# Kernel tuning notes

Measured on AMD Instinct MI355X. Metric: run time of the kernel, lower is better.

The kernel has to match this reference:

```python
import jax, jax.numpy as jnp
import numpy as np

B, S, H = 32, 2048, 1024

def setup_inputs() -> dict:
    key = jax.random.key(0)
    k1, k2, k3, k4, k5, k6 = jax.random.split(key, 6)
    return {
        "query": jax.random.normal(k1, (B, 1, H), dtype=jnp.float32),
        "keys": jax.random.normal(k2, (B, S, H), dtype=jnp.float32),
        "mask": jax.random.randint(k3, (B, S, 1), 0, 2, dtype=jnp.int32),
        "W1": jax.random.normal(k4, (H, H), dtype=jnp.float32) * (1.0 / np.sqrt(H)),
        "W2": jax.random.normal(k5, (H, H), dtype=jnp.float32) * (1.0 / np.sqrt(H)),
        "V": jax.random.normal(k6, (H, 1), dtype=jnp.float32) * (1.0 / np.sqrt(H)),
    }

def reference(query, keys, mask, W1, W2, V):
    # W1(keys): [B,S,H]; W2(query): [B,1,H] broadcasts over S (== expand in torch)
    proj = jnp.tanh(jnp.einsum('bsh,hd->bsd', keys, W1) +
                    jnp.einsum('bqh,hd->bqd', query, W2))
    scores = jnp.einsum('bsd,do->bso', proj, V)          # [B,S,1]
    scores = jnp.where(mask == 0, jnp.float32(-1e9), scores)
    scores = scores[..., 0]                               # [B,S]
    attn = jax.nn.softmax(scores, axis=1)                 # [B,S]
    context = jnp.einsum('bs,bsh->bh', attn, keys)        # [B,H]
    return (context, attn)
```

## Files before the change

kernel.cpp:

```cpp
#include <hip/hip_runtime.h>

typedef float  f32x4 __attribute__((ext_vector_type(4)));
typedef short  s16x8 __attribute__((ext_vector_type(8)));
typedef short  s16x4 __attribute__((ext_vector_type(4)));
typedef unsigned short u16;

#define HDIM 1024
#define BATCH 32
#define SEQ 2048
#define NROWS (BATCH*SEQ)

#define BM 256
#define BN 256
#define BK 32
#define NKT (HDIM/BK)

#define GLD16(gp, lp) __builtin_amdgcn_global_load_lds( \
    (const __attribute__((address_space(1))) void*)(gp), \
    (__attribute__((address_space(3))) void*)(lp), 16, 0, 0)

#define VMCNT(n) asm volatile("s_waitcnt vmcnt(" #n ")" ::: "memory")
#define LGKM0    asm volatile("s_waitcnt lgkmcnt(0)" ::: "memory")
#define BARRIER  asm volatile("s_barrier" ::: "memory")
#define SCHEDB   __builtin_amdgcn_sched_barrier(0)

__device__ __forceinline__ u16 f2bf(float f){
    unsigned u = __float_as_uint(f);
    u = u + 0x7FFFu + ((u >> 16) & 1u);
    return (u16)(u >> 16);
}

__device__ __forceinline__ float tanh_fast(float x){
    float e = __builtin_amdgcn_exp2f(x * 2.885390082f);
    return 1.0f - 2.0f * __builtin_amdgcn_rcpf(e + 1.0f);
}

__global__ __launch_bounds__(256) void k_mask(const int* __restrict__ mask,
                                              int* __restrict__ cnt,
                                              int* __restrict__ idx,
                                              int* __restrict__ pos){
    int b = blockIdx.x, t = threadIdx.x;
    const int* mb = mask + (size_t)b * SEQ;
    int f[8], s = 0;
#pragma unroll
    for (int i = 0; i < 8; ++i){ f[i] = (mb[t * 8 + i] != 0); s += f[i]; }
    __shared__ int ps[256];
    ps[t] = s;
    __syncthreads();
    for (int off = 1; off < 256; off <<= 1){
        int v = (t >= off) ? ps[t - off] : 0;
        __syncthreads();
        ps[t] += v;
        __syncthreads();
    }
    int run = ps[t] - s;
    if (t == 255) cnt[b] = ps[255];
#pragma unroll
    for (int i = 0; i < 8; ++i){
        int so = t * 8 + i;
        if (f[i]){
            idx[(size_t)b * SEQ + run] = so;
            pos[(size_t)b * SEQ + so]  = run;
            ++run;
        }
    }
}

__global__ __launch_bounds__(256) void k_gather(const float* __restrict__ keys,
                                                const int* __restrict__ cnt,
                                                const int* __restrict__ idx,
                                                u16* __restrict__ keysbf){
    int blk = blockIdx.x;
    int b = blk >> 8, chunk = blk & 255;
    int n = cnt[b];
    int base = chunk * 8;
    if (base >= n) return;
    int t = threadIdx.x;
    int j = t >> 5, l = t & 31;
    int slot = base + j;
    if (slot >= n) return;
    int orig = idx[(size_t)b * SEQ + slot];
    const float* src = keys + ((size_t)b * SEQ + orig) * HDIM + l * 4;
    u16* dst = keysbf + ((size_t)b * SEQ + slot) * HDIM + l * 4;
#pragma unroll
    for (int i = 0; i < 8; ++i){
        f32x4 v = *(const f32x4*)(src + i * 128);
        s16x4 o;
        o[0] = (short)f2bf(v.x); o[1] = (short)f2bf(v.y);
        o[2] = (short)f2bf(v.z); o[3] = (short)f2bf(v.w);
        *(s16x4*)(dst + i * 128) = o;
    }
}

__global__ __launch_bounds__(256) void k_w1t(const float* __restrict__ W1,
                                             u16* __restrict__ W1T){
    __shared__ u16 t[64][65];
    int blk = blockIdx.x;
    int bh = blk >> 4, bd = blk & 15;
    int h0 = bh * 64, d0 = bd * 64;
    int tid = threadIdx.x;
    int lh = tid >> 4, ld = (tid & 15) * 4;
#pragma unroll
    for (int i = 0; i < 4; ++i){
        int hh = lh + i * 16;
        f32x4 v = *(const f32x4*)&W1[(size_t)(h0 + hh) * HDIM + d0 + ld];
        t[hh][ld + 0] = f2bf(v.x);
        t[hh][ld + 1] = f2bf(v.y);
        t[hh][ld + 2] = f2bf(v.z);
        t[hh][ld + 3] = f2bf(v.w);
    }
    __syncthreads();
    int wv = tid >> 6, ln = tid & 63;
#pragma unroll
    for (int i = 0; i < 16; ++i){
        int d = i * 4 + wv;
        W1T[(size_t)(d0 + d) * HDIM + h0 + ln] = t[ln][d];
    }
}

__global__ __launch_bounds__(256) void k_qproj(const float* __restrict__ query,
                                               const float* __restrict__ W2,
                                               float* __restrict__ qproj){
    int b = blockIdx.x >> 4, dc = blockIdx.x & 15;
    int t = threadIdx.x;
    int dl = t & 63, hq = t >> 6;
    int d = dc * 64 + dl;
    const float* q = query + (size_t)b * HDIM;
    float acc = 0.f;
#pragma unroll 8
    for (int h = hq * 256; h < hq * 256 + 256; ++h)
        acc += q[h] * W2[(size_t)h * HDIM + d];
    __shared__ float red[4][64];
    red[hq][dl] = acc;
    __syncthreads();
    if (hq == 0)
        qproj[(size_t)b * HDIM + d] = red[0][dl] + red[1][dl] + red[2][dl] + red[3][dl];
}

__global__ __launch_bounds__(512, 2) void k_score(const u16* __restrict__ keysbf,
                                                  const u16* __restrict__ W1T,
                                                  const float* __restrict__ qproj,
                                                  const float* __restrict__ V,
                                                  const int* __restrict__ cnt,
                                                  float* __restrict__ spart){
    int bid = blockIdx.x;
    int lid = (bid & 7) * 128 + (bid >> 3);
    int mt  = lid >> 2;
    int nt  = lid & 3;
    int b_idx = mt >> 3;
    if ((mt & 7) * 256 >= cnt[b_idx]) return;

    __shared__ u16 As[2][BM * BK];
    __shared__ u16 Bs[2][BM * BK];

    int tid  = threadIdx.x;
    int lane = tid & 63, wave = tid >> 6;
    int wm = wave >> 2, wn = wave & 3;
    int g  = lane >> 4, q = lane & 15;

    int sr = tid >> 2, sl = tid & 3;
    int ch = sl ^ ((sr >> 1) & 3);
    const u16* asrc = keysbf + (size_t)(mt * BM + sr) * HDIM + ch * 8;
    const u16* bsrc = W1T    + (size_t)(nt * BN + sr) * HDIM + ch * 8;
    int dst = tid * 8;

    auto stage = [&](int buf, int kt){
        int ko = kt * BK;
        GLD16(asrc + ko,               &As[buf][dst]);
        GLD16(asrc + ko + 128 * HDIM,  &As[buf][dst + 128 * BK]);
        GLD16(bsrc + ko,               &Bs[buf][dst]);
        GLD16(bsrc + ko + 128 * HDIM,  &Bs[buf][dst + 128 * BK]);
    };

    int slotx = (q >> 1) & 3;
    int rslot = (g ^ slotx) * 8;
    int aoff = (wm * 128 + q) * BK + rslot;
    int boff = (wn * 64 + q) * BK + rslot;

    f32x4 acc[8][4];
#pragma unroll
    for (int m = 0; m < 8; ++m)
#pragma unroll
        for (int n = 0; n < 4; ++n) acc[m][n] = 0.f;

    stage(0, 0);
    stage(1, 1);
    VMCNT(4);
    SCHEDB;
    BARRIER;
    SCHEDB;

    for (int kt = 0; kt < NKT; ++kt){
        int cur = kt & 1;
        s16x8 af[8], bq[4];
#pragma unroll
        for (int m = 0; m < 8; ++m) af[m] = *(const s16x8*)&As[cur][aoff + m * 16 * BK];
#pragma unroll
        for (int n = 0; n < 4; ++n) bq[n] = *(const s16x8*)&Bs[cur][boff + n * 16 * BK];

        __builtin_amdgcn_s_setprio(1);
#pragma unroll
        for (int m = 0; m < 8; ++m)
#pragma unroll
            for (int n = 0; n < 4; ++n)
                acc[m][n] = __builtin_amdgcn_mfma_f32_16x16x32_bf16(af[m], bq[n], acc[m][n], 0, 0, 0);
        __builtin_amdgcn_s_setprio(0);

        SCHEDB;
        LGKM0;
        BARRIER;
        SCHEDB;
        stage(cur, (kt + 2 < NKT) ? kt + 2 : NKT - 1);
        VMCNT(4);
        SCHEDB;
        BARRIER;
        SCHEDB;
    }
    VMCNT(0);

    float Vn[4], Qn[4];
#pragma unroll
    for (int n = 0; n < 4; ++n){
        int D = nt * BN + wn * 64 + n * 16 + q;
        Vn[n] = V[D];
        Qn[n] = qproj[(size_t)b_idx * HDIM + D];
    }
#pragma unroll
    for (int m = 0; m < 8; ++m){
#pragma unroll
        for (int r = 0; r < 4; ++r){
            float s = 0.f;
#pragma unroll
            for (int n = 0; n < 4; ++n){
                float x = acc[m][n][r] + Qn[n];
                s += Vn[n] * tanh_fast(x);
            }
            s += __shfl_xor(s, 1);
            s += __shfl_xor(s, 2);
            s += __shfl_xor(s, 4);
            s += __shfl_xor(s, 8);
            if (q == 0){
                int R = mt * BM + wm * 128 + m * 16 + g * 4 + r;
                spart[(size_t)R * 16 + nt * 4 + wn] = s;
            }
        }
    }
}

__global__ __launch_bounds__(256) void k_softmax(const float* __restrict__ spart,
                                                 const int* __restrict__ mask,
                                                 const int* __restrict__ pos,
                                                 float* __restrict__ attn){
    int b = blockIdx.x;
    int tid = threadIdx.x;
    int lane = tid & 63, wv = tid >> 6;
    __shared__ float redmx[4];
    __shared__ float redsm[4];

    float sc[8];
#pragma unroll
    for (int i = 0; i < 8; ++i){
        int s = i * 256 + tid;
        int mk = mask[(size_t)b * SEQ + s];
        if (mk != 0){
            int p = pos[(size_t)b * SEQ + s];
            const f32x4* pp = (const f32x4*)&spart[((size_t)b * SEQ + p) * 16];
            f32x4 v0 = pp[0], v1 = pp[1], v2 = pp[2], v3 = pp[3];
            sc[i] = (v0.x + v0.y + v0.z + v0.w) + (v1.x + v1.y + v1.z + v1.w)
                  + (v2.x + v2.y + v2.z + v2.w) + (v3.x + v3.y + v3.z + v3.w);
        } else {
            sc[i] = -1e9f;
        }
    }
    float mx = sc[0];
#pragma unroll
    for (int i = 1; i < 8; ++i) mx = fmaxf(mx, sc[i]);
#pragma unroll
    for (int o = 32; o >= 1; o >>= 1) mx = fmaxf(mx, __shfl_xor(mx, o));
    if (lane == 0) redmx[wv] = mx;
    __syncthreads();
    mx = fmaxf(fmaxf(redmx[0], redmx[1]), fmaxf(redmx[2], redmx[3]));

    float ex[8], ssum = 0.f;
#pragma unroll
    for (int i = 0; i < 8; ++i){
        ex[i] = __builtin_amdgcn_exp2f((sc[i] - mx) * 1.4426950408889634f);
        ssum += ex[i];
    }
#pragma unroll
    for (int o = 32; o >= 1; o >>= 1) ssum += __shfl_xor(ssum, o);
    if (lane == 0) redsm[wv] = ssum;
    __syncthreads();
    ssum = redsm[0] + redsm[1] + redsm[2] + redsm[3];
    float inv = 1.0f / ssum;
#pragma unroll
    for (int i = 0; i < 8; ++i)
        attn[(size_t)b * SEQ + i * 256 + tid] = ex[i] * inv;
}

__global__ __launch_bounds__(256) void k_ctxpart(const u16* __restrict__ keysbf,
                                                 const float* __restrict__ attn,
                                                 const int* __restrict__ cnt,
                                                 const int* __restrict__ idx,
                                                 float* __restrict__ cpart){
    int blk = blockIdx.x;
    int b = blk >> 5, scn = blk & 31;
    int t = threadIdx.x;
    int n = cnt[b];
    int lim = n - scn * 64;
    if (lim > 64) lim = 64;
    f32x4 acc = 0.f;
    const s16x4* kp = (const s16x4*)(keysbf + (size_t)(b * SEQ + scn * 64) * HDIM) + t;
    const int* ip = idx + (size_t)b * SEQ + scn * 64;
    const float* ab = attn + (size_t)b * SEQ;
    for (int s = 0; s < lim; ++s){
        float a = ab[ip[s]];
        s16x4 kv = kp[(size_t)s * 256];
        f32x4 kf;
        kf.x = __uint_as_float((unsigned)(unsigned short)kv[0] << 16);
        kf.y = __uint_as_float((unsigned)(unsigned short)kv[1] << 16);
        kf.z = __uint_as_float((unsigned)(unsigned short)kv[2] << 16);
        kf.w = __uint_as_float((unsigned)(unsigned short)kv[3] << 16);
        acc += a * kf;
    }
    *(f32x4*)&cpart[(size_t)(b * 32 + scn) * HDIM + t * 4] = acc;
}

__global__ __launch_bounds__(256) void k_ctxred(const float* __restrict__ cpart,
                                                float* __restrict__ ctx){
    int idx = blockIdx.x * 256 + threadIdx.x;
    int b = idx >> 10, h = idx & 1023;
    float s = 0.f;
#pragma unroll
    for (int sc = 0; sc < 32; ++sc)
        s += cpart[(size_t)(b * 32 + sc) * HDIM + h];
    ctx[idx] = s;
}

extern "C" void kernel_launch(void* const* d_in, const int* in_sizes, int n_in,
                              void* d_out, int out_size, void* d_ws, size_t ws_size,
                              hipStream_t stream){
    (void)in_sizes; (void)n_in; (void)out_size; (void)ws_size;
    const float* query = (const float*)d_in[0];
    const float* keys  = (const float*)d_in[1];
    const int*   mask  = (const int*)d_in[2];
    const float* W1    = (const float*)d_in[3];
    const float* W2    = (const float*)d_in[4];
    const float* V     = (const float*)d_in[5];

    float* ctx_out  = (float*)d_out;
    float* attn_out = ctx_out + BATCH * HDIM;

    char* ws = (char*)d_ws;
    u16*   W1T   = (u16*)ws;
    float* qproj = (float*)(ws + (2u << 20));
    int*   cnt   = (int*)  (ws + (2u << 20) + (256u << 10));
    int*   idx   = (int*)  (ws + (2u << 20) + (512u << 10));
    int*   pos   = (int*)  (ws + (3u << 20));
    float* spart = (float*)(ws + (4u << 20));
    float* cpart = spart;
    u16*   keysbf= (u16*)(ws + (9u << 20));

    k_w1t    <<<dim3(256),  dim3(256), 0, stream>>>(W1, W1T);
    k_qproj  <<<dim3(512),  dim3(256), 0, stream>>>(query, W2, qproj);
    k_mask   <<<dim3(32),   dim3(256), 0, stream>>>(mask, cnt, idx, pos);
    k_gather <<<dim3(8192), dim3(256), 0, stream>>>(keys, cnt, idx, keysbf);
    k_score  <<<dim3(1024), dim3(512), 0, stream>>>(keysbf, W1T, qproj, V, cnt, spart);
    k_softmax<<<dim3(32),   dim3(256), 0, stream>>>(spart, mask, pos, attn_out);
    k_ctxpart<<<dim3(1024), dim3(256), 0, stream>>>(keysbf, attn_out, cnt, idx, cpart);
    k_ctxred <<<dim3(128),  dim3(256), 0, stream>>>(cpart, ctx_out);
}
```

Measured before the change: 202.9 us.

## Compact unmasked rows across groups of four batches and merge setup kernels

Masked-row compaction now runs over groups of four batches (8192 rows) instead of per batch, so the score GEMM's 256-row tiles are packed across batch boundaries. This leaves fewer partially filled tiles. The score epilogue picks each row's query projection by comparing against per-batch offsets, and ctxpart uses those offsets to find each batch's segment. The W1 transpose, query projection and mask scan are also fused into one launch, which removes two kernel launches. The cost is extra per-element select logic in the epilogue and a somewhat more complex index scheme.

Measured after the change: 196.9 us (median of 2 runs). 3.0% less time.

```diff
diff --git a/kernel.cpp b/kernel.cpp
--- a/kernel.cpp
+++ b/kernel.cpp
@@ -1,6 +1,7 @@
 #include <hip/hip_runtime.h>
 
 typedef float  f32x4 __attribute__((ext_vector_type(4)));
+typedef int    i32x4 __attribute__((ext_vector_type(4)));
 typedef short  s16x8 __attribute__((ext_vector_type(8)));
 typedef short  s16x4 __attribute__((ext_vector_type(4)));
 typedef unsigned short u16;
@@ -9,6 +10,8 @@
 #define BATCH 32
 #define SEQ 2048
 #define NROWS (BATCH*SEQ)
+#define GSEQ 8192
+#define NGRP 8
 
 #define BM 256
 #define BN 256
@@ -35,53 +38,107 @@
     return 1.0f - 2.0f * __builtin_amdgcn_rcpf(e + 1.0f);
 }
 
-__global__ __launch_bounds__(256) void k_mask(const int* __restrict__ mask,
-                                              int* __restrict__ cnt,
-                                              int* __restrict__ idx,
-                                              int* __restrict__ pos){
-    int b = blockIdx.x, t = threadIdx.x;
-    const int* mb = mask + (size_t)b * SEQ;
-    int f[8], s = 0;
-#pragma unroll
-    for (int i = 0; i < 8; ++i){ f[i] = (mb[t * 8 + i] != 0); s += f[i]; }
+__global__ __launch_bounds__(256) void k_setup(const float* __restrict__ W1,
+                                               u16* __restrict__ W1T,
+                                               const float* __restrict__ query,
+                                               const float* __restrict__ W2,
+                                               float* __restrict__ qproj,
+                                               const int* __restrict__ mask,
+                                               int* __restrict__ cnt4,
+                                               int* __restrict__ off,
+                                               int* __restrict__ idx,
+                                               int* __restrict__ pos){
+    __shared__ u16 tsh[64][65];
+    __shared__ float red[4][64];
     __shared__ int ps[256];
-    ps[t] = s;
-    __syncthreads();
-    for (int off = 1; off < 256; off <<= 1){
-        int v = (t >= off) ? ps[t - off] : 0;
+    int blk = blockIdx.x;
+    int tid = threadIdx.x;
+
+    if (blk < 256){
+        int bh = blk >> 4, bd = blk & 15;
+        int h0 = bh * 64, d0 = bd * 64;
+        int lh = tid >> 4, ld = (tid & 15) * 4;
+#pragma unroll
+        for (int i = 0; i < 4; ++i){
+            int hh = lh + i * 16;
+            f32x4 v = *(const f32x4*)&W1[(size_t)(h0 + hh) * HDIM + d0 + ld];
+            tsh[hh][ld + 0] = f2bf(v.x);
+            tsh[hh][ld + 1] = f2bf(v.y);
+            tsh[hh][ld + 2] = f2bf(v.z);
+            tsh[hh][ld + 3] = f2bf(v.w);
+        }
         __syncthreads();
-        ps[t] += v;
+        int wv = tid >> 6, ln = tid & 63;
+#pragma unroll
+        for (int i = 0; i < 16; ++i){
+            int d = i * 4 + wv;
+            W1T[(size_t)(d0 + d) * HDIM + h0 + ln] = tsh[ln][d];
+        }
+    } else if (blk < 768){
+        int blk2 = blk - 256;
+        int b = blk2 >> 4, dc = blk2 & 15;
+        int dl = tid & 63, hq = tid >> 6;
+        int d = dc * 64 + dl;
+        const float* q = query + (size_t)b * HDIM;
+        float acc = 0.f;
+#pragma unroll 8
+        for (int h = hq * 256; h < hq * 256 + 256; ++h)
+            acc += q[h] * W2[(size_t)h * HDIM + d];
+        red[hq][dl] = acc;
         __syncthreads();
-    }
-    int run = ps[t] - s;
-    if (t == 255) cnt[b] = ps[255];
-#pragma unroll
-    for (int i = 0; i < 8; ++i){
-        int so = t * 8 + i;
-        if (f[i]){
-            idx[(size_t)b * SEQ + run] = so;
-            pos[(size_t)b * SEQ + so]  = run;
-            ++run;
+        if (hq == 0)
+            qproj[(size_t)b * HDIM + d] = red[0][dl] + red[1][dl] + red[2][dl] + red[3][dl];
+    } else {
+        int g = blk - 768;
+        const int* mb = mask + (size_t)g * GSEQ;
+        unsigned bits = 0;
+#pragma unroll
+        for (int i = 0; i < 8; ++i){
+            i32x4 v = ((const i32x4*)mb)[tid * 8 + i];
+            bits |= (unsigned)(v.x != 0) << (i * 4 + 0);
+            bits |= (unsigned)(v.y != 0) << (i * 4 + 1);
+            bits |= (unsigned)(v.z != 0) << (i * 4 + 2);
+            bits |= (unsigned)(v.w != 0) << (i * 4 + 3);
+        }
+        int s = __popc(bits);
+        ps[tid] = s;
+        __syncthreads();
+        for (int o = 1; o < 256; o <<= 1){
+            int v = (tid >= o) ? ps[tid - o] : 0;
+            __syncthreads();
+            ps[tid] += v;
+            __syncthreads();
+        }
+        int run = ps[tid] - s;
+        if (tid == 255) cnt4[g] = ps[255];
+        if ((tid & 63) == 0) off[g * 4 + (tid >> 6)] = run;
+        for (int i = 0; i < 32; ++i){
+            if ((bits >> i) & 1u){
+                int slot = run + __popc(bits & ((1u << i) - 1u));
+                int so = tid * 32 + i;
+                idx[(size_t)g * GSEQ + slot] = so;
+                pos[(size_t)g * GSEQ + so]  = slot;
+            }
         }
     }
 }
 
 __global__ __launch_bounds__(256) void k_gather(const float* __restrict__ keys,
-                                                const int* __restrict__ cnt,
+                                                const int* __restrict__ cnt4,
                                                 const int* __restrict__ idx,
                                                 u16* __restrict__ keysbf){
     int blk = blockIdx.x;
-    int b = blk >> 8, chunk = blk & 255;
-    int n = cnt[b];
+    int g = blk >> 10, chunk = blk & 1023;
+    int n = cnt4[g];
     int base = chunk * 8;
     if (base >= n) return;
     int t = threadIdx.x;
     int j = t >> 5, l = t & 31;
     int slot = base + j;
     if (slot >= n) return;
-    int orig = idx[(size_t)b * SEQ + slot];
-    const float* src = keys + ((size_t)b * SEQ + orig) * HDIM + l * 4;
-    u16* dst = keysbf + ((size_t)b * SEQ + slot) * HDIM + l * 4;
+    int orig = idx[(size_t)g * GSEQ + slot];
+    const float* src = keys + ((size_t)g * GSEQ + orig) * HDIM + l * 4;
+    u16* dst = keysbf + ((size_t)g * GSEQ + slot) * HDIM + l * 4;
 #pragma unroll
     for (int i = 0; i < 8; ++i){
         f32x4 v = *(const f32x4*)(src + i * 128);
@@ -92,63 +149,20 @@
     }
 }
 
-__global__ __launch_bounds__(256) void k_w1t(const float* __restrict__ W1,
-                                             u16* __restrict__ W1T){
-    __shared__ u16 t[64][65];
-    int blk = blockIdx.x;
-    int bh = blk >> 4, bd = blk & 15;
-    int h0 = bh * 64, d0 = bd * 64;
-    int tid = threadIdx.x;
-    int lh = tid >> 4, ld = (tid & 15) * 4;
-#pragma unroll
-    for (int i = 0; i < 4; ++i){
-        int hh = lh + i * 16;
-        f32x4 v = *(const f32x4*)&W1[(size_t)(h0 + hh) * HDIM + d0 + ld];
-        t[hh][ld + 0] = f2bf(v.x);
-        t[hh][ld + 1] = f2bf(v.y);
-        t[hh][ld + 2] = f2bf(v.z);
-        t[hh][ld + 3] = f2bf(v.w);
-    }
-    __syncthreads();
-    int wv = tid >> 6, ln = tid & 63;
-#pragma unroll
-    for (int i = 0; i < 16; ++i){
-        int d = i * 4 + wv;
-        W1T[(size_t)(d0 + d) * HDIM + h0 + ln] = t[ln][d];
-    }
-}
-
-__global__ __launch_bounds__(256) void k_qproj(const float* __restrict__ query,
-                                               const float* __restrict__ W2,
-                                               float* __restrict__ qproj){
-    int b = blockIdx.x >> 4, dc = blockIdx.x & 15;
-    int t = threadIdx.x;
-    int dl = t & 63, hq = t >> 6;
-    int d = dc * 64 + dl;
-    const float* q = query + (size_t)b * HDIM;
-    float acc = 0.f;
-#pragma unroll 8
-    for (int h = hq * 256; h < hq * 256 + 256; ++h)
-        acc += q[h] * W2[(size_t)h * HDIM + d];
-    __shared__ float red[4][64];
-    red[hq][dl] = acc;
-    __syncthreads();
-    if (hq == 0)
-        qproj[(size_t)b * HDIM + d] = red[0][dl] + red[1][dl] + red[2][dl] + red[3][dl];
-}
-
 __global__ __launch_bounds__(512, 2) void k_score(const u16* __restrict__ keysbf,
                                                   const u16* __restrict__ W1T,
                                                   const float* __restrict__ qproj,
                                                   const float* __restrict__ V,
-                                                  const int* __restrict__ cnt,
+                                                  const int* __restrict__ cnt4,
+                                                  const int* __restrict__ off,
                                                   float* __restrict__ spart){
     int bid = blockIdx.x;
     int lid = (bid & 7) * 128 + (bid >> 3);
-    int mt  = lid >> 2;
-    int nt  = lid & 3;
-    int b_idx = mt >> 3;
-    if ((mt & 7) * 256 >= cnt[b_idx]) return;
+    int gb  = lid >> 7;
+    int r7  = lid & 127;
+    int mtl = r7 >> 2;
+    int nt  = r7 & 3;
+    if (mtl * 256 >= cnt4[gb]) return;
 
     __shared__ u16 As[2][BM * BK];
     __shared__ u16 Bs[2][BM * BK];
@@ -156,11 +170,11 @@
     int tid  = threadIdx.x;
     int lane = tid & 63, wave = tid >> 6;
     int wm = wave >> 2, wn = wave & 3;
-    int g  = lane >> 4, q = lane & 15;
+    int lg = lane >> 4, q = lane & 15;
 
     int sr = tid >> 2, sl = tid & 3;
     int ch = sl ^ ((sr >> 1) & 3);
-    const u16* asrc = keysbf + (size_t)(mt * BM + sr) * HDIM + ch * 8;
+    const u16* asrc = keysbf + ((size_t)gb * GSEQ + mtl * BM + sr) * HDIM + ch * 8;
     const u16* bsrc = W1T    + (size_t)(nt * BN + sr) * HDIM + ch * 8;
     int dst = tid * 8;
 
@@ -173,7 +187,7 @@
     };
 
     int slotx = (q >> 1) & 3;
-    int rslot = (g ^ slotx) * 8;
+    int rslot = (lg ^ slotx) * 8;
     int aoff = (wm * 128 + q) * BK + rslot;
     int boff = (wn * 64 + q) * BK + rslot;
 
@@ -218,31 +232,38 @@
     }
     VMCNT(0);
 
-    float Vn[4], Qn[4];
+    int o1 = off[gb * 4 + 1], o2 = off[gb * 4 + 2], o3 = off[gb * 4 + 3];
+    float Vn[4], Q0[4], Q1[4], Q2[4], Q3[4];
 #pragma unroll
     for (int n = 0; n < 4; ++n){
         int D = nt * BN + wn * 64 + n * 16 + q;
         Vn[n] = V[D];
-        Qn[n] = qproj[(size_t)b_idx * HDIM + D];
+        Q0[n] = qproj[(size_t)(gb * 4 + 0) * HDIM + D];
+        Q1[n] = qproj[(size_t)(gb * 4 + 1) * HDIM + D];
+        Q2[n] = qproj[(size_t)(gb * 4 + 2) * HDIM + D];
+        Q3[n] = qproj[(size_t)(gb * 4 + 3) * HDIM + D];
     }
 #pragma unroll
     for (int m = 0; m < 8; ++m){
 #pragma unroll
         for (int r = 0; r < 4; ++r){
+            int loc = mtl * BM + wm * 128 + m * 16 + lg * 4 + r;
             float s = 0.f;
 #pragma unroll
             for (int n = 0; n < 4; ++n){
-                float x = acc[m][n][r] + Qn[n];
+                float Qn = Q0[n];
+                Qn = (loc >= o1) ? Q1[n] : Qn;
+                Qn = (loc >= o2) ? Q2[n] : Qn;
+                Qn = (loc >= o3) ? Q3[n] : Qn;
+                float x = acc[m][n][r] + Qn;
                 s += Vn[n] * tanh_fast(x);
             }
             s += __shfl_xor(s, 1);
             s += __shfl_xor(s, 2);
             s += __shfl_xor(s, 4);
             s += __shfl_xor(s, 8);
-            if (q == 0){
-                int R = mt * BM + wm * 128 + m * 16 + g * 4 + r;
-                spart[(size_t)R * 16 + nt * 4 + wn] = s;
-            }
+            if (q == 0)
+                spart[((size_t)gb * GSEQ + loc) * 16 + nt * 4 + wn] = s;
         }
     }
 }
@@ -252,6 +273,7 @@
                                                  const int* __restrict__ pos,
                                                  float* __restrict__ attn){
     int b = blockIdx.x;
+    int gb = b >> 2;
     int tid = threadIdx.x;
     int lane = tid & 63, wv = tid >> 6;
     __shared__ float redmx[4];
@@ -264,7 +286,7 @@
         int mk = mask[(size_t)b * SEQ + s];
         if (mk != 0){
             int p = pos[(size_t)b * SEQ + s];
-            const f32x4* pp = (const f32x4*)&spart[((size_t)b * SEQ + p) * 16];
+            const f32x4* pp = (const f32x4*)&spart[((size_t)gb * GSEQ + p) * 16];
             f32x4 v0 = pp[0], v1 = pp[1], v2 = pp[2], v3 = pp[3];
             sc[i] = (v0.x + v0.y + v0.z + v0.w) + (v1.x + v1.y + v1.z + v1.w)
                   + (v2.x + v2.y + v2.z + v2.w) + (v3.x + v3.y + v3.z + v3.w);
@@ -300,21 +322,26 @@
 
 __global__ __launch_bounds__(256) void k_ctxpart(const u16* __restrict__ keysbf,
                                                  const float* __restrict__ attn,
-                                                 const int* __restrict__ cnt,
+                                                 const int* __restrict__ cnt4,
+                                                 const int* __restrict__ off,
                                                  const int* __restrict__ idx,
                                                  float* __restrict__ cpart){
     int blk = blockIdx.x;
     int b = blk >> 5, scn = blk & 31;
+    int gb = b >> 2, j = b & 3;
+    int oj  = off[gb * 4 + j];
+    int oj1 = (j < 3) ? off[gb * 4 + j + 1] : cnt4[gb];
+    int nb  = oj1 - oj;
+    int lim = nb - scn * 64;
+    if (lim > 64) lim = 64;
     int t = threadIdx.x;
-    int n = cnt[b];
-    int lim = n - scn * 64;
-    if (lim > 64) lim = 64;
     f32x4 acc = 0.f;
-    const s16x4* kp = (const s16x4*)(keysbf + (size_t)(b * SEQ + scn * 64) * HDIM) + t;
-    const int* ip = idx + (size_t)b * SEQ + scn * 64;
-    const float* ab = attn + (size_t)b * SEQ;
+    size_t base = (size_t)gb * GSEQ + oj + scn * 64;
+    const s16x4* kp = (const s16x4*)(keysbf + base * HDIM) + t;
+    const int* ip = idx + base;
+    const float* ab = attn;
     for (int s = 0; s < lim; ++s){
-        float a = ab[ip[s]];
+        float a = ab[(size_t)gb * GSEQ + ip[s]];
         s16x4 kv = kp[(size_t)s * 256];
         f32x4 kf;
         kf.x = __uint_as_float((unsigned)(unsigned short)kv[0] << 16);
@@ -328,13 +355,13 @@
 
 __global__ __launch_bounds__(256) void k_ctxred(const float* __restrict__ cpart,
                                                 float* __restrict__ ctx){
-    int idx = blockIdx.x * 256 + threadIdx.x;
-    int b = idx >> 10, h = idx & 1023;
+    int id = blockIdx.x * 256 + threadIdx.x;
+    int b = id >> 10, h = id & 1023;
     float s = 0.f;
 #pragma unroll
     for (int sc = 0; sc < 32; ++sc)
         s += cpart[(size_t)(b * 32 + sc) * HDIM + h];
-    ctx[idx] = s;
+    ctx[id] = s;
 }
 
 extern "C" void kernel_launch(void* const* d_in, const int* in_sizes, int n_in,
@@ -354,19 +381,21 @@
     char* ws = (char*)d_ws;
     u16*   W1T   = (u16*)ws;
     float* qproj = (float*)(ws + (2u << 20));
-    int*   cnt   = (int*)  (ws + (2u << 20) + (256u << 10));
+    int*   cnt4  = (int*)  (ws + (2u << 20) + (128u << 10));
+    int*   off   = (int*)  (ws + (2u << 20) + (132u << 10));
     int*   idx   = (int*)  (ws + (2u << 20) + (512u << 10));
     int*   pos   = (int*)  (ws + (3u << 20));
     float* spart = (float*)(ws + (4u << 20));
     float* cpart = spart;
     u16*   keysbf= (u16*)(ws + (9u << 20));
 
-    k_w1t    <<<dim3(256),  dim3(256), 0, stream>>>(W1, W1T);
-    k_qproj  <<<dim3(512),  dim3(256), 0, stream>>>(query, W2, qproj);
-    k_mask   <<<dim3(32),   dim3(256), 0, stream>>>(mask, cnt, idx, pos);
-    k_gather <<<dim3(8192), dim3(256), 0, stream>>>(keys, cnt, idx, keysbf);
-    k_score  <<<dim3(1024), dim3(512), 0, stream>>>(keysbf, W1T, qproj, V, cnt, spart);
+    k_setup  <<<dim3(776),  dim3(256), 0, stream>>>(W1, W1T, query, W2, qproj,
+                                                    mask, cnt4, off, idx, pos);
+    k_gather <<<dim3(8192), dim3(256), 0, stream>>>(keys, cnt4, idx, keysbf);
+    k_score  <<<dim3(1024), dim3(512), 0, stream>>>(keysbf, W1T, qproj, V,
+                                                    cnt4, off, spart);
     k_softmax<<<dim3(32),   dim3(256), 0, stream>>>(spart, mask, pos, attn_out);
-    k_ctxpart<<<dim3(1024), dim3(256), 0, stream>>>(keysbf, attn_out, cnt, idx, cpart);
+    k_ctxpart<<<dim3(1024), dim3(256), 0, stream>>>(keysbf, attn_out, cnt4, off,
+                                                    idx, cpart);
     k_ctxred <<<dim3(128),  dim3(256), 0, stream>>>(cpart, ctx_out);
 }
```
